# Kernel optimization log

Hardware: AMD Instinct MI355X
Metric: run time of the kernel (lower is better)

The kernel has to match this reference:

```python
import jax, jax.numpy as jnp
import numpy as np

N = 50000          # nodes
E = 800000         # edges (before self loops)
IC = 16            # in_channels; pos = x[:, :3]
H = (64, 64, 128, 128)
OUT = 8
INS = (IC, IC + H[0], IC + H[0] + H[1], IC + H[0] + H[1] + H[2])


def _lin_w(k, fi, fo):
    s = 1.0 / np.sqrt(fi)
    return jax.random.uniform(k, (fi, fo), minval=-s, maxval=s, dtype=jnp.float32)


def setup_inputs() -> dict:
    key = jax.random.key(0)
    ks = jax.random.split(key, 64)
    inp = {
        "x": jax.random.normal(ks[0], (N, IC), dtype=jnp.float32),
        "edge_index": jax.random.randint(ks[1], (2, E), 0, N, dtype=jnp.int32),
    }
    ki = 2
    for i, (fi, fo) in enumerate(zip(INS, H), start=1):
        inp[f"Wl{i}"] = _lin_w(ks[ki], fi, fo); ki += 1   # lin (values), no bias
        inp[f"Ws{i}"] = _lin_w(ks[ki], fi, fo); ki += 1   # lin_src, no bias
        inp[f"Wd{i}"] = _lin_w(ks[ki], fi, fo); ki += 1   # lin_dst, no bias
        inp[f"Wp{i}"] = _lin_w(ks[ki], 3, fo); ki += 1    # pos_nn = Linear(3, fo)
        inp[f"bp{i}"] = jnp.zeros((fo,), jnp.float32)
    inp["Wm1"] = _lin_w(ks[ki], IC + sum(H), 64); ki += 1
    inp["bm1"] = jnp.zeros((64,), jnp.float32)
    inp["Wm2"] = _lin_w(ks[ki], 64, OUT); ki += 1
    inp["bm2"] = jnp.zeros((OUT,), jnp.float32)
    return inp


def _pt_conv(h, pos, src, dst, Wl, Ws, Wd, Wp, bp, n):
    """PointTransformerConv: per-channel softmax attention over incoming edges."""
    a_src = h @ Ws                               # alpha_j part  [N, F]
    a_dst = h @ Wd                               # alpha_i part  [N, F]
    v = h @ Wl                                   # values        [N, F]
    delta = (pos[dst] - pos[src]) @ Wp + bp      # pos_nn(pos_i - pos_j)  [E, F]
    alpha = a_dst[dst] - a_src[src] + delta      # [E, F]
    m = jax.ops.segment_max(alpha, dst, num_segments=n)
    ea = jnp.exp(alpha - m[dst])
    s = jax.ops.segment_sum(ea, dst, num_segments=n)
    attn = ea / s[dst]                           # segment softmax (self loops -> s > 0)
    return jax.ops.segment_sum(attn * (v[src] + delta), dst, num_segments=n)


def reference(x, edge_index, Wl1, Ws1, Wd1, Wp1, bp1, Wl2, Ws2, Wd2, Wp2, bp2,
              Wl3, Ws3, Wd3, Wp3, bp3, Wl4, Ws4, Wd4, Wp4, bp4, Wm1, bm1, Wm2, bm2):
    n = x.shape[0]
    pos = x[:, :3]
    loop = jnp.arange(n, dtype=edge_index.dtype)
    src = jnp.concatenate([edge_index[0], loop])  # PyG add_self_loops (default True)
    dst = jnp.concatenate([edge_index[1], loop])
    lrelu = lambda v: jax.nn.leaky_relu(v, 0.01)
    x1 = lrelu(_pt_conv(x, pos, src, dst, Wl1, Ws1, Wd1, Wp1, bp1, n))
    h2 = jnp.concatenate([x, x1], 1)
    x2 = lrelu(_pt_conv(h2, pos, src, dst, Wl2, Ws2, Wd2, Wp2, bp2, n))
    h3 = jnp.concatenate([x, x1, x2], 1)
    x3 = lrelu(_pt_conv(h3, pos, src, dst, Wl3, Ws3, Wd3, Wp3, bp3, n))
    h4 = jnp.concatenate([x, x1, x2, x3], 1)
    x4 = lrelu(_pt_conv(h4, pos, src, dst, Wl4, Ws4, Wd4, Wp4, bp4, n))
    out = jnp.concatenate([x, x1, x2, x3, x4], 1)  # dropout = identity (eval mode)
    out = out @ Wm1 + bm1
    return out @ Wm2 + bm2
```

## Files before the change

### kernel.cpp

```cpp
#include <hip/hip_runtime.h>
#include <hip/hip_bf16.h>
#include <hip/hip_fp16.h>
#include <math.h>

#define N_NODES 50000
#define N_EDGES 800000
#define ET (N_EDGES + N_NODES)
#define HTOT 400
#define SENTINEL 50000u

#define SCAN_CHUNK 1024
#define NSCB ((N_NODES + SCAN_CHUNK - 1) / SCAN_CHUNK)

typedef __attribute__((ext_vector_type(4))) float f32x4;
typedef __attribute__((ext_vector_type(8))) short bf16x8;

static const int INS_h[4] = {16, 80, 144, 272};
static const int K32_h[4] = {32, 96, 160, 288};
static const int HO_h[4]  = {64, 64, 128, 128};

#define LOG2E_F 1.4426950408889634f


struct PrepArgs {
    const float* x; __hip_bfloat16* h; int* deg;
    const float* Ws0; const float* Wl0;
    const float* Ws1; const float* Wl1;
    const float* Ws2; const float* Wl2;
    const float* Ws3; const float* Wl3;
    const float* Wm1;
    __hip_bfloat16* Wt0; __hip_bfloat16* Wt1; __hip_bfloat16* Wt2;
    __hip_bfloat16* Wt3; __hip_bfloat16* WtF;
    ushort* av;
};

__device__ inline void concat1(const float* __restrict__ W0, const float* __restrict__ W1,
                               int K, int K32, int fo, __hip_bfloat16* __restrict__ Wt, int i) {
    int c = i / K32, kk = i - c * K32;
    float v = 0.f;
    if (kk < K) v = (c < fo) ? W0[kk * fo + c] : W1[kk * fo + (c - fo)];
    Wt[i] = __float2bfloat16(v);
}

#define PREP_TOTAL 1008080

__global__ __launch_bounds__(256) void prep_kernel(PrepArgs a) {
    int i = blockIdx.x * 256 + threadIdx.x;
    if (i < 800000) {
        int n = i >> 4, c = i & 15;
        a.h[n * HTOT + c] = __float2bfloat16(a.x[i]);
        return;
    }
    i -= 800000;
    if (i < 50000) { a.deg[i] = 0; return; }
    i -= 50000;
    if (i < 4096)  { concat1(a.Ws0, a.Wl0, 16, 32, 64, a.Wt0, i); return; }
    i -= 4096;
    if (i < 12288) { concat1(a.Ws1, a.Wl1, 80, 96, 64, a.Wt1, i); return; }
    i -= 12288;
    if (i < 40960) { concat1(a.Ws2, a.Wl2, 144, 160, 128, a.Wt2, i); return; }
    i -= 40960;
    if (i < 73728) { concat1(a.Ws3, a.Wl3, 272, 288, 128, a.Wt3, i); return; }
    i -= 73728;
    if (i < 26624) {
        int c = i / 416, kk = i - c * 416;
        float v = (kk < 400) ? a.Wm1[kk * 64 + c] : 0.f;
        a.WtF[i] = __float2bfloat16(v);
        return;
    }
    i -= 26624;
    if (i < 384) {
        if (i < 128) a.av[50000 * 128 + i] = (i < 64)  ? 0xFC00 : 0;
        else { int j = i - 128; a.av[50000 * 256 + j] = (j < 128) ? 0xFC00 : 0; }
    }
}


__global__ void hist_kernel(const int* __restrict__ ei, int* __restrict__ deg) {
    int e = blockIdx.x * blockDim.x + threadIdx.x;
    if (e >= ET) return;
    int dst = (e < N_EDGES) ? ei[N_EDGES + e] : (e - N_EDGES);
    atomicAdd(&deg[dst], 1);
}

__global__ __launch_bounds__(256) void scan_p1(const int* __restrict__ deg,
                                               int* __restrict__ bsum) {
    __shared__ int red[256];
    const int b = blockIdx.x, t = threadIdx.x;
    const int base = b * SCAN_CHUNK + t * 4;
    int s = 0;
#pragma unroll
    for (int j = 0; j < 4; ++j) {
        int i = base + j;
        if (i < N_NODES) s += deg[i];
    }
    red[t] = s;
    __syncthreads();
    for (int off = 128; off > 0; off >>= 1) {
        if (t < off) red[t] += red[t + off];
        __syncthreads();
    }
    if (t == 0) bsum[b] = red[0];
}

__global__ __launch_bounds__(256) void scan_p3(const int* __restrict__ deg,
                                               const int* __restrict__ bsum,
                                               int* __restrict__ row_ptr,
                                               int* __restrict__ cursor) {
    __shared__ int ts[256];
    __shared__ int sb[2];
    const int b = blockIdx.x, t = threadIdx.x;
    if (t < 64) {
        int v = (t < NSCB) ? bsum[t] : 0;
        int inc = v;
#pragma unroll
        for (int off = 1; off < 64; off <<= 1) {
            int u = __shfl_up(inc, off);
            if (t >= off) inc += u;
        }
        if (t == b) sb[0] = inc - v;
        if (t == 63) sb[1] = inc;
    }
    const int base = b * SCAN_CHUNK + t * 4;
    int v[4];
    int s = 0;
#pragma unroll
    for (int j = 0; j < 4; ++j) {
        int i = base + j;
        v[j] = (i < N_NODES) ? deg[i] : 0;
        s += v[j];
    }
    ts[t] = s;
    __syncthreads();
    for (int off = 1; off < 256; off <<= 1) {
        int u = (t >= off) ? ts[t - off] : 0;
        __syncthreads();
        ts[t] += u;
        __syncthreads();
    }
    int excl = sb[0] + ts[t] - s;
#pragma unroll
    for (int j = 0; j < 4; ++j) {
        int i = base + j;
        if (i < N_NODES) {
            row_ptr[i] = excl;
            cursor[i] = excl;
            excl += v[j];
        }
    }
    if (b == 0 && t == 0) row_ptr[N_NODES] = sb[1];
}

__global__ void scatter_kernel(const int* __restrict__ ei, const float* __restrict__ x,
                               int* __restrict__ cursor, uint2* __restrict__ edata) {
    int e = blockIdx.x * blockDim.x + threadIdx.x;
    if (e >= ET) return;
    int src, dst;
    if (e < N_EDGES) { src = ei[e]; dst = ei[N_EDGES + e]; }
    else             { src = dst = e - N_EDGES; }
    int p = atomicAdd(&cursor[dst], 1);
    float4 pd = *(const float4*)&x[dst * 16];
    float4 ps = *(const float4*)&x[src * 16];
    __half dxh = __float2half(pd.x - ps.x);
    __half dyh = __float2half(pd.y - ps.y);
    __half dzh = __float2half(pd.z - ps.z);
    uint w0 = (uint)src | ((uint)__half_as_ushort(dzh) << 16);
    __half2 xy;
    xy.x = dxh; xy.y = dyh;
    edata[p] = make_uint2(w0, *(uint*)&xy);
}


template <bool FUSE>
__global__ __launch_bounds__(256) void gemm3_kernel(
    const __hip_bfloat16* __restrict__ A, int lda,
    const __hip_bfloat16* __restrict__ Wt, int K32,
    const float* __restrict__ bias,
    __half* __restrict__ av, int fo,
    int M, int K, int GXP,
    const float* __restrict__ W2, const float* __restrict__ b2,
    float* __restrict__ out) {
    __shared__ float smemf[9728];
    ushort* sA = (ushort*)smemf;
    ushort* sB = (ushort*)smemf + 10240;
    const int t = threadIdx.x;
    const int bid = blockIdx.x;
    const int gxp = bid % GXP;
    const int gy = bid / GXP;
    const int r0 = gxp * 128, c0 = gy * 64;
    const int w = t >> 6, lane = t & 63;
    const int l15 = lane & 15, l4 = lane >> 4;

    f32x4 acc[2][4];
#pragma unroll
    for (int i = 0; i < 2; ++i)
#pragma unroll
        for (int j = 0; j < 4; ++j) acc[i][j] = (f32x4){0.f, 0.f, 0.f, 0.f};

    const int sr = t >> 2, sq = (t & 3) * 8;
    const int ar1 = min(r0 + sr, M - 1), ar2 = min(r0 + sr + 64, M - 1);
    const size_t a1b = (size_t)ar1 * lda, a2b = (size_t)ar2 * lda;
    const size_t wb = (size_t)(c0 + sr) * K32;
    const int nk = K32 >> 5;

    uint4 ga0, ga1, gb;
    const uint4 z4 = {0u, 0u, 0u, 0u};
    {
        const int kk = sq;
        const bool ok = kk < K;
        ga0 = ok ? *(const uint4*)(A + a1b + kk) : z4;
        ga1 = ok ? *(const uint4*)(A + a2b + kk) : z4;
        gb  = *(const uint4*)(Wt + wb + kk);
        *(uint4*)(sA + sr * 40 + sq) = ga0;
        *(uint4*)(sA + (sr + 64) * 40 + sq) = ga1;
        *(uint4*)(sB + sr * 40 + sq) = gb;
    }
    __syncthreads();

    int buf = 0;
    for (int kc = 0; kc < nk; ++kc) {
        const bool nx = (kc + 1) < nk;
        if (nx) {
            const int kk = (kc + 1) * 32 + sq;
            const bool ok = kk < K;
            ga0 = ok ? *(const uint4*)(A + a1b + kk) : z4;
            ga1 = ok ? *(const uint4*)(A + a2b + kk) : z4;
            gb  = *(const uint4*)(Wt + wb + kk);
        }
        const ushort* bA = sA + buf * 5120 + w * 1280;
        const ushort* bB = sB + buf * 2560;
        bf16x8 af[2], bfr[4];
#pragma unroll
        for (int i = 0; i < 2; ++i)
            af[i] = *(const bf16x8*)(bA + (i * 16 + l15) * 40 + l4 * 8);
#pragma unroll
        for (int j = 0; j < 4; ++j)
            bfr[j] = *(const bf16x8*)(bB + (j * 16 + l15) * 40 + l4 * 8);
#pragma unroll
        for (int i = 0; i < 2; ++i)
#pragma unroll
            for (int j = 0; j < 4; ++j)
                acc[i][j] = __builtin_amdgcn_mfma_f32_16x16x32_bf16(af[i], bfr[j], acc[i][j], 0, 0, 0);
        if (nx) {
            const int ob = buf ^ 1;
            *(uint4*)(sA + ob * 5120 + sr * 40 + sq) = ga0;
            *(uint4*)(sA + ob * 5120 + (sr + 64) * 40 + sq) = ga1;
            *(uint4*)(sB + ob * 2560 + sr * 40 + sq) = gb;
        }
        __syncthreads();
        buf ^= 1;
    }

    if (!FUSE) {
        const int n2 = 2 * fo;
#pragma unroll
        for (int i = 0; i < 2; ++i)
#pragma unroll
            for (int j = 0; j < 4; ++j)
#pragma unroll
                for (int p = 0; p < 4; ++p) {
                    int row = r0 + w * 32 + i * 16 + l4 * 4 + p;
                    int col = c0 + j * 16 + l15;
                    if (row < M) {
                        float vv = acc[i][j][p];
                        if (col < fo) vv *= -LOG2E_F;
                        av[(size_t)row * n2 + col] = __float2half(vv);
                    }
                }
    } else {
#pragma unroll
        for (int i = 0; i < 2; ++i)
#pragma unroll
            for (int j = 0; j < 4; ++j)
#pragma unroll
                for (int p = 0; p < 4; ++p) {
                    int lrow = w * 32 + i * 16 + l4 * 4 + p;
                    int col = j * 16 + l15;
                    smemf[lrow * 68 + col] = acc[i][j][p] + bias[col];
                }
        smemf[8704 + t] = W2[t];
        smemf[8704 + 256 + t] = W2[256 + t];
        __syncthreads();
        const int row = t >> 1, oc = (t & 1) * 4;
        f32x4 o = *(const f32x4*)&b2[oc];
#pragma unroll 8
        for (int k = 0; k < 64; ++k) {
            float a = smemf[row * 68 + k];
            o += a * *(const f32x4*)&smemf[8704 + k * 8 + oc];
        }
        const int grow = r0 + row;
        if (grow < M) *(f32x4*)&out[(size_t)grow * 8 + oc] = o;
    }
}


__device__ inline __half2 h2e2(__half2 a) {
    __half2 r;
    r.x = hexp2(__low2half(a));
    r.y = hexp2(__high2half(a));
    return r;
}

template <int LPE>
__global__ __launch_bounds__(256) void attn_kernel(
    __hip_bfloat16* __restrict__ h,
    const __half* __restrict__ av,
    const float* __restrict__ Wp, const float* __restrict__ bp,
    const int* __restrict__ rowp, const uint2* __restrict__ edata,
    int colbase) {
    constexpr int FO = 8 * LPE;
    constexpr int SLOTS = 64 / LPE;
    const int wid = (blockIdx.x * (int)blockDim.x + (int)threadIdx.x) >> 6;
    if (wid >= N_NODES) return;
    const int lane = threadIdx.x & 63;
    const int e = lane / LPE, lp = lane % LPE;
    const int cb = lp * 8;

    __half2 wp0h[4], wp1h[4], wp2h[4], bph[4];
#pragma unroll
    for (int jj = 0; jj < 4; ++jj) {
        int c = cb + 2 * jj;
        wp0h[jj] = __floats2half2_rn(Wp[c], Wp[c + 1]);
        wp1h[jj] = __floats2half2_rn(Wp[FO + c], Wp[FO + c + 1]);
        wp2h[jj] = __floats2half2_rn(Wp[2 * FO + c], Wp[2 * FO + c + 1]);
        bph[jj]  = __floats2half2_rn(bp[c], bp[c + 1]);
    }
    __half2 s2[4], n2v[4];
    const __half2 hz = __float2half2_rn(0.f);
#pragma unroll
    for (int j = 0; j < 4; ++j) { s2[j] = hz; n2v[j] = hz; }

    const uint* avu = (const uint*)av;
    const __half2 L2E = __float2half2_rn(LOG2E_F);
    const int beg = rowp[wid], end = rowp[wid + 1], last = end - 1;

    auto ld = [&](int b, uint2& ed, uint4& a4, uint4& v4) {
        ed = edata[min(b + e, last)];
        const uint src = (b + e < end) ? (ed.x & 0xFFFFu) : SENTINEL;
        const uint* rb = avu + (size_t)src * FO + (cb >> 1);
        a4 = *(const uint4*)rb;
        v4 = *(const uint4*)(rb + FO / 2);
    };
    auto compute = [&](const uint2& ed, const uint4& a4, const uint4& v4) {
        __half2 dz2 = __half2half2(__ushort_as_half((ushort)(ed.x >> 16)));
        __half2 dxy = *(const __half2*)&ed.y;
        __half2 dx2 = __half2half2(__low2half(dxy));
        __half2 dy2 = __half2half2(__high2half(dxy));
        const uint* ap = (const uint*)&a4;
        const uint* vp = (const uint*)&v4;
#pragma unroll
        for (int jj = 0; jj < 4; ++jj) {
            __half2 d  = __hfma2(dx2, wp0h[jj], __hfma2(dy2, wp1h[jj], __hfma2(dz2, wp2h[jj], bph[jj])));
            __half2 a2 = __hfma2(d, L2E, *(const __half2*)&ap[jj]);
            __half2 vd = __hadd2(*(const __half2*)&vp[jj], d);
            __half2 p2 = h2e2(a2);
            s2[jj] = __hadd2(s2[jj], p2);
            n2v[jj] = __hfma2(p2, vd, n2v[jj]);
        }
    };

    uint2 edX, edY;
    uint4 aX, vX, aY, vY;
    int nit = (end - beg + SLOTS - 1) / SLOTS;
    nit = (nit + 1) & ~1;
    ld(beg, edX, aX, vX);
    for (int k = 0; k < nit; k += 2) {
        ld(beg + (k + 1) * SLOTS, edY, aY, vY);
        compute(edX, aX, vX);
        ld(beg + (k + 2) * SLOTS, edX, aX, vX);
        compute(edY, aY, vY);
    }

    float s[8], num[8];
#pragma unroll
    for (int jj = 0; jj < 4; ++jj) {
        s[2 * jj]       = __half2float(__low2half(s2[jj]));
        s[2 * jj + 1]   = __half2float(__high2half(s2[jj]));
        num[2 * jj]     = __half2float(__low2half(n2v[jj]));
        num[2 * jj + 1] = __half2float(__high2half(n2v[jj]));
    }
#pragma unroll
    for (int j = 0; j < 8; ++j) {
#pragma unroll
        for (int off = LPE; off < 64; off <<= 1) {
            s[j] += __shfl_xor(s[j], off);
            num[j] += __shfl_xor(num[j], off);
        }
    }
    if (e == 0) {
        ushort o[8];
#pragma unroll
        for (int j = 0; j < 8; ++j) {
            float xi = num[j] / s[j];
            xi = xi > 0.f ? xi : 0.01f * xi;
            __hip_bfloat16 b = __float2bfloat16(xi);
            o[j] = *(ushort*)&b;
        }
        ushort* dst = (ushort*)&h[(size_t)wid * HTOT + colbase + cb];
        *(uint4*)dst = *(uint4*)o;
    }
}


extern "C" void kernel_launch(void* const* d_in, const int* in_sizes, int n_in,
                              void* d_out, int out_size, void* d_ws, size_t ws_size,
                              hipStream_t stream) {
    const float* x = (const float*)d_in[0];
    const int* ei = (const int*)d_in[1];
    const float *Wl[4], *Ws[4], *Wp[4], *bp[4];
    for (int i = 0; i < 4; ++i) {
        Wl[i] = (const float*)d_in[2 + 5 * i];
        Ws[i] = (const float*)d_in[3 + 5 * i];
        Wp[i] = (const float*)d_in[5 + 5 * i];
        bp[i] = (const float*)d_in[6 + 5 * i];
    }
    const float* Wm1 = (const float*)d_in[22];
    const float* bm1 = (const float*)d_in[23];
    const float* Wm2 = (const float*)d_in[24];
    const float* bm2 = (const float*)d_in[25];
    float* out = (float*)d_out;

    char* ws = (char*)d_ws;
    size_t off = 0;
    auto alloc = [&](size_t bytes) -> void* {
        void* p = ws + off;
        off += (bytes + 255) & ~(size_t)255;
        return p;
    };
    __hip_bfloat16* h = (__hip_bfloat16*)alloc((size_t)N_NODES * HTOT * 2);
    __half* av = (__half*)alloc((size_t)(N_NODES + 1) * 256 * 2);
    __hip_bfloat16* Wt0 = (__hip_bfloat16*)alloc((size_t)4096 * 2);
    __hip_bfloat16* Wt1 = (__hip_bfloat16*)alloc((size_t)12288 * 2);
    __hip_bfloat16* Wt2 = (__hip_bfloat16*)alloc((size_t)40960 * 2);
    __hip_bfloat16* Wt3 = (__hip_bfloat16*)alloc((size_t)73728 * 2);
    __hip_bfloat16* WtF = (__hip_bfloat16*)alloc((size_t)26624 * 2);
    int* deg = (int*)alloc((size_t)N_NODES * 4);
    int* rowp = (int*)alloc((size_t)(N_NODES + 1) * 4);
    int* cursor = (int*)alloc((size_t)N_NODES * 4);
    int* bsum = (int*)alloc((size_t)(NSCB + 1) * 4);
    uint2* edata = (uint2*)alloc((size_t)ET * 8);
    (void)ws_size; (void)n_in; (void)in_sizes; (void)out_size;

    PrepArgs pa;
    pa.x = x; pa.h = h; pa.deg = deg;
    pa.Ws0 = Ws[0]; pa.Wl0 = Wl[0];
    pa.Ws1 = Ws[1]; pa.Wl1 = Wl[1];
    pa.Ws2 = Ws[2]; pa.Wl2 = Wl[2];
    pa.Ws3 = Ws[3]; pa.Wl3 = Wl[3];
    pa.Wm1 = Wm1;
    pa.Wt0 = Wt0; pa.Wt1 = Wt1; pa.Wt2 = Wt2; pa.Wt3 = Wt3; pa.WtF = WtF;
    pa.av = (ushort*)av;
    prep_kernel<<<(PREP_TOTAL + 255) / 256, 256, 0, stream>>>(pa);

    hist_kernel<<<(ET + 255) / 256, 256, 0, stream>>>(ei, deg);
    scan_p1<<<NSCB, 256, 0, stream>>>(deg, bsum);
    scan_p3<<<NSCB, 256, 0, stream>>>(deg, bsum, rowp, cursor);
    scatter_kernel<<<(ET + 255) / 256, 256, 0, stream>>>(ei, x, cursor, edata);

    const int M = N_NODES;
    const int GXP = (((M + 127) / 128 + 7) / 8) * 8;
    const int nbn = (N_NODES + 3) / 4;
    __hip_bfloat16* Wts[4] = {Wt0, Wt1, Wt2, Wt3};
    for (int L = 0; L < 4; ++L) {
        const int K = INS_h[L], K32 = K32_h[L], fo = HO_h[L], n2 = 2 * fo;
        gemm3_kernel<false><<<GXP * (n2 / 64), 256, 0, stream>>>(
            h, HTOT, Wts[L], K32, nullptr, av, fo, M, K, GXP, nullptr, nullptr, nullptr);
        if (fo == 64)
            attn_kernel<8><<<nbn, 256, 0, stream>>>(h, av, Wp[L], bp[L], rowp, edata, K);
        else
            attn_kernel<16><<<nbn, 256, 0, stream>>>(h, av, Wp[L], bp[L], rowp, edata, K);
    }
    gemm3_kernel<true><<<GXP, 256, 0, stream>>>(h, HTOT, WtF, 416, bm1,
                                                nullptr, 0, M, 400, GXP, Wm2, bm2, out);
}
```

Measured before the change: 360.6 us.

## Stage GEMM av output through LDS, prepack pos weights, simplify attn loop

The GEMM epilogue now writes fp16 results into shared memory and then emits coalesced 16-byte row stores, replacing scattered 2-byte global stores. Positional weights and bias are pre-converted once to packed half2 in the prep kernel, so attn threads load them with four vector loads instead of per-element float loads and conversions. The attention edge loop becomes a single-stage software pipeline with exact trip count, dropping the forced even iteration count. This adds an extra __syncthreads and LDS traffic in the GEMM epilogue.

```diff
diff --git a/kernel.cpp b/kernel.cpp
--- a/kernel.cpp
+++ b/kernel.cpp
@@ -32,6 +32,11 @@
     __hip_bfloat16* Wt0; __hip_bfloat16* Wt1; __hip_bfloat16* Wt2;
     __hip_bfloat16* Wt3; __hip_bfloat16* WtF;
     ushort* av;
+    const float* Wp0; const float* bp0;
+    const float* Wp1; const float* bp1;
+    const float* Wp2; const float* bp2;
+    const float* Wp3; const float* bp3;
+    uint* wph0; uint* wph1; uint* wph2; uint* wph3;
 };
 
 __device__ inline void concat1(const float* __restrict__ W0, const float* __restrict__ W1,
@@ -42,7 +47,7 @@
     Wt[i] = __float2bfloat16(v);
 }
 
-#define PREP_TOTAL 1008080
+#define PREP_TOTAL 1008848
 
 __global__ __launch_bounds__(256) void prep_kernel(PrepArgs a) {
     int i = blockIdx.x * 256 + threadIdx.x;
@@ -72,6 +77,23 @@
     if (i < 384) {
         if (i < 128) a.av[50000 * 128 + i] = (i < 64)  ? 0xFC00 : 0;
         else { int j = i - 128; a.av[50000 * 256 + j] = (j < 128) ? 0xFC00 : 0; }
+        return;
+    }
+    i -= 384;
+    if (i < 768) {
+        const float* Wp; const float* bpp; uint* dst; int fo; int q = i;
+        if (q < 128)      { Wp = a.Wp0; bpp = a.bp0; dst = a.wph0; fo = 64; }
+        else if (q < 256) { q -= 128; Wp = a.Wp1; bpp = a.bp1; dst = a.wph1; fo = 64; }
+        else if (q < 512) { q -= 256; Wp = a.Wp2; bpp = a.bp2; dst = a.wph2; fo = 128; }
+        else              { q -= 512; Wp = a.Wp3; bpp = a.bp3; dst = a.wph3; fo = 128; }
+        int hf = fo >> 1;
+        int arr = q / hf, pr = q - arr * hf;
+        int c = 2 * pr;
+        float v0, v1;
+        if (arr < 3) { v0 = Wp[arr * fo + c]; v1 = Wp[arr * fo + c + 1]; }
+        else         { v0 = bpp[c]; v1 = bpp[c + 1]; }
+        __half2 hh = __floats2half2_rn(v0, v1);
+        dst[q] = *reinterpret_cast<uint*>(&hh);
     }
 }
 
@@ -253,20 +275,33 @@
 
     if (!FUSE) {
         const int n2 = 2 * fo;
+        ushort* st = (ushort*)smemf;
 #pragma unroll
         for (int i = 0; i < 2; ++i)
 #pragma unroll
             for (int j = 0; j < 4; ++j)
 #pragma unroll
                 for (int p = 0; p < 4; ++p) {
-                    int row = r0 + w * 32 + i * 16 + l4 * 4 + p;
+                    int lrow = w * 32 + i * 16 + l4 * 4 + p;
                     int col = c0 + j * 16 + l15;
-                    if (row < M) {
-                        float vv = acc[i][j][p];
-                        if (col < fo) vv *= -LOG2E_F;
-                        av[(size_t)row * n2 + col] = __float2half(vv);
-                    }
+                    float vv = acc[i][j][p];
+                    if (col < fo) vv *= -LOG2E_F;
+                    __half hv = __float2half(vv);
+                    st[lrow * 68 + j * 16 + l15] = __half_as_ushort(hv);
                 }
+        __syncthreads();
+        const int row = t >> 1, seg = (t & 1) * 32;
+        const int grow = r0 + row;
+        if (grow < M) {
+            __half* dst = av + (size_t)grow * n2 + c0 + seg;
+#pragma unroll
+            for (int u = 0; u < 4; ++u) {
+                uint2 qa = *(const uint2*)(st + row * 68 + seg + 8 * u);
+                uint2 qb = *(const uint2*)(st + row * 68 + seg + 8 * u + 4);
+                uint4 q4 = make_uint4(qa.x, qa.y, qb.x, qb.y);
+                *(uint4*)(dst + 8 * u) = q4;
+            }
+        }
     } else {
 #pragma unroll
         for (int i = 0; i < 2; ++i)
@@ -305,7 +340,7 @@
 __global__ __launch_bounds__(256) void attn_kernel(
     __hip_bfloat16* __restrict__ h,
     const __half* __restrict__ av,
-    const float* __restrict__ Wp, const float* __restrict__ bp,
+    const uint* __restrict__ wph,
     const int* __restrict__ rowp, const uint2* __restrict__ edata,
     int colbase) {
     constexpr int FO = 8 * LPE;
@@ -316,15 +351,15 @@
     const int e = lane / LPE, lp = lane % LPE;
     const int cb = lp * 8;
 
-    __half2 wp0h[4], wp1h[4], wp2h[4], bph[4];
-#pragma unroll
-    for (int jj = 0; jj < 4; ++jj) {
-        int c = cb + 2 * jj;
-        wp0h[jj] = __floats2half2_rn(Wp[c], Wp[c + 1]);
-        wp1h[jj] = __floats2half2_rn(Wp[FO + c], Wp[FO + c + 1]);
-        wp2h[jj] = __floats2half2_rn(Wp[2 * FO + c], Wp[2 * FO + c + 1]);
-        bph[jj]  = __floats2half2_rn(bp[c], bp[c + 1]);
-    }
+    uint4 w0 = *(const uint4*)(wph + 0 * (FO / 2) + lp * 4);
+    uint4 w1 = *(const uint4*)(wph + 1 * (FO / 2) + lp * 4);
+    uint4 w2 = *(const uint4*)(wph + 2 * (FO / 2) + lp * 4);
+    uint4 wb4 = *(const uint4*)(wph + 3 * (FO / 2) + lp * 4);
+    const __half2* wp0h = (const __half2*)&w0;
+    const __half2* wp1h = (const __half2*)&w1;
+    const __half2* wp2h = (const __half2*)&w2;
+    const __half2* bph  = (const __half2*)&wb4;
+
     __half2 s2[4], n2v[4];
     const __half2 hz = __float2half2_rn(0.f);
 #pragma unroll
@@ -334,6 +369,8 @@
     const __half2 L2E = __float2half2_rn(LOG2E_F);
     const int beg = rowp[wid], end = rowp[wid + 1], last = end - 1;
 
+    uint2 ed_c, ed_n;
+    uint4 a_c, v_c, a_n, v_n;
     auto ld = [&](int b, uint2& ed, uint4& a4, uint4& v4) {
         ed = edata[min(b + e, last)];
         const uint src = (b + e < end) ? (ed.x & 0xFFFFu) : SENTINEL;
@@ -359,16 +396,11 @@
         }
     };
 
-    uint2 edX, edY;
-    uint4 aX, vX, aY, vY;
-    int nit = (end - beg + SLOTS - 1) / SLOTS;
-    nit = (nit + 1) & ~1;
-    ld(beg, edX, aX, vX);
-    for (int k = 0; k < nit; k += 2) {
-        ld(beg + (k + 1) * SLOTS, edY, aY, vY);
-        compute(edX, aX, vX);
-        ld(beg + (k + 2) * SLOTS, edX, aX, vX);
-        compute(edY, aY, vY);
+    ld(beg, ed_c, a_c, v_c);
+    for (int base = beg; base < end; base += SLOTS) {
+        ld(base + SLOTS, ed_n, a_n, v_n);
+        compute(ed_c, a_c, v_c);
+        ed_c = ed_n; a_c = a_n; v_c = v_n;
     }
 
     float s[8], num[8];
@@ -434,6 +466,10 @@
     __hip_bfloat16* Wt2 = (__hip_bfloat16*)alloc((size_t)40960 * 2);
     __hip_bfloat16* Wt3 = (__hip_bfloat16*)alloc((size_t)73728 * 2);
     __hip_bfloat16* WtF = (__hip_bfloat16*)alloc((size_t)26624 * 2);
+    uint* wph0 = (uint*)alloc((size_t)128 * 4);
+    uint* wph1 = (uint*)alloc((size_t)128 * 4);
+    uint* wph2 = (uint*)alloc((size_t)256 * 4);
+    uint* wph3 = (uint*)alloc((size_t)256 * 4);
     int* deg = (int*)alloc((size_t)N_NODES * 4);
     int* rowp = (int*)alloc((size_t)(N_NODES + 1) * 4);
     int* cursor = (int*)alloc((size_t)N_NODES * 4);
@@ -450,6 +486,11 @@
     pa.Wm1 = Wm1;
     pa.Wt0 = Wt0; pa.Wt1 = Wt1; pa.Wt2 = Wt2; pa.Wt3 = Wt3; pa.WtF = WtF;
     pa.av = (ushort*)av;
+    pa.Wp0 = Wp[0]; pa.bp0 = bp[0];
+    pa.Wp1 = Wp[1]; pa.bp1 = bp[1];
+    pa.Wp2 = Wp[2]; pa.bp2 = bp[2];
+    pa.Wp3 = Wp[3]; pa.bp3 = bp[3];
+    pa.wph0 = wph0; pa.wph1 = wph1; pa.wph2 = wph2; pa.wph3 = wph3;
     prep_kernel<<<(PREP_TOTAL + 255) / 256, 256, 0, stream>>>(pa);
 
     hist_kernel<<<(ET + 255) / 256, 256, 0, stream>>>(ei, deg);
@@ -461,14 +502,15 @@
     const int GXP = (((M + 127) / 128 + 7) / 8) * 8;
     const int nbn = (N_NODES + 3) / 4;
     __hip_bfloat16* Wts[4] = {Wt0, Wt1, Wt2, Wt3};
+    uint* wphs[4] = {wph0, wph1, wph2, wph3};
     for (int L = 0; L < 4; ++L) {
         const int K = INS_h[L], K32 = K32_h[L], fo = HO_h[L], n2 = 2 * fo;
         gemm3_kernel<false><<<GXP * (n2 / 64), 256, 0, stream>>>(
             h, HTOT, Wts[L], K32, nullptr, av, fo, M, K, GXP, nullptr, nullptr, nullptr);
         if (fo == 64)
-            attn_kernel<8><<<nbn, 256, 0, stream>>>(h, av, Wp[L], bp[L], rowp, edata, K);
+            attn_kernel<8><<<nbn, 256, 0, stream>>>(h, av, wphs[L], rowp, edata, K);
         else
-            attn_kernel<16><<<nbn, 256, 0, stream>>>(h, av, Wp[L], bp[L], rowp, edata, K);
+            attn_kernel<16><<<nbn, 256, 0, stream>>>(h, av, wphs[L], rowp, edata, K);
     }
     gemm3_kernel<true><<<GXP, 256, 0, stream>>>(h, HTOT, WtF, 416, bm1,
                                                 nullptr, 0, M, 400, GXP, Wm2, bm2, out);
```

New measurement: 361.6 us. No clear change (+0.3%).
